# Performance work log

Hardware: AMD Instinct MI355X
Metric: run time of the kernel (lower is better)

## Reference

```python
import jax, jax.numpy as jnp
import numpy as np

NU, NI, D, C, V, E, L = 100000, 50000, 128, 5, 200000, 200000, 10


def setup_inputs() -> dict:
    key = jax.random.key(0)
    ks = jax.random.split(key, 16)
    s = lambda fan_in: 1.0 / np.sqrt(fan_in)
    return {
        "urf": jax.random.normal(ks[0], (NU, D), jnp.float32),
        "irf": jax.random.normal(ks[1], (NI, D), jnp.float32),
        "utf": jax.random.normal(ks[2], (NU, D), jnp.float32),
        "itf": jax.random.normal(ks[3], (NI, D), jnp.float32),
        "w1r": jax.random.normal(ks[4], (2 * D, D), jnp.float32) * s(2 * D),
        "w2r": jax.random.normal(ks[5], (D, D), jnp.float32) * s(D),
        "w1t": jax.random.normal(ks[6], (2 * D, D), jnp.float32) * s(2 * D),
        "w2t": jax.random.normal(ks[7], (D, D), jnp.float32) * s(D),
        "wp": jax.random.normal(ks[8], (D, C), jnp.float32) * s(D),
        "emb": jax.random.normal(ks[9], (V, D), jnp.float32),
        "src": jax.random.randint(ks[10], (E,), 0, NU, jnp.int32),
        "dst": jax.random.randint(ks[11], (E,), 0, NI, jnp.int32),
        "sentence_id": jax.random.randint(ks[12], (E, L), 0, V, jnp.int32),
        "neg_sid": jax.random.randint(ks[13], (E, L), 1, V, jnp.int32),
    }


def _review_feature(emb, sid):
    # masked mean-pool of sentence embeddings: [E, L] -> [E, D]
    length = (sid > 0).astype(jnp.float32).sum(axis=-1, keepdims=True) + 1e-9
    return emb[sid].sum(axis=-2) / length


def reference(urf, irf, utf, itf, w1r, w2r, w1t, w2t, wp, emb,
              src, dst, sentence_id, neg_sid):
    # edge-wise gather of src (user) / dst (item) features + concat  [E, 2D]
    rf = jnp.concatenate([urf[src], irf[dst]], axis=1)
    rh = jax.nn.relu(rf @ w1r) @ w2r                      # rating_linear  [E, D]
    pr = rh @ wp                                          # rating_predictor [E, C]
    tf = jnp.concatenate([utf[src], itf[dst]], axis=1)
    th = jax.nn.relu(tf @ w1t) @ w2t + rh                 # topic_linear + residual
    pos_review = _review_feature(emb, sentence_id)        # [E, D]
    neg_review = _review_feature(emb, neg_sid)            # [E, D]
    pos_score = (th * pos_review).sum(axis=1)             # [E]
    neg_score = (th * neg_review).sum(axis=1)
    loss = -jax.nn.log_sigmoid(pos_score - neg_score)     # -log(sigmoid(pos-neg))
    return pr, loss.mean(), loss.mean()
```

## Files before the change

### kernel.cpp

```cpp
#include <hip/hip_runtime.h>

#define NU_ 100000
#define NI_ 50000
#define D_  128
#define C_  5
#define V_  200000
#define E_  200000
#define L_  10

typedef __bf16 bf16x8 __attribute__((ext_vector_type(8)));
typedef unsigned short u16;
typedef u16 u16x8 __attribute__((ext_vector_type(8)));
typedef float f32x4 __attribute__((ext_vector_type(4)));

#define W1R_OFF 0
#define W2R_OFF 32768
#define W1T_OFF 49152
#define W2T_OFF 81920
#define WTOT    98304
#define EMB_BYTE_OFF (256 * 1024)
#define EMB_ELEMS    (V_ * D_)

__device__ __forceinline__ u16 f2bf(float x) {
    union { float f; unsigned int u; } v; v.f = x;
    unsigned int u = v.u;
    return (u16)((u + 0x7FFFu + ((u >> 16) & 1u)) >> 16);
}
__device__ __forceinline__ float bfhi(unsigned int u) {
    union { unsigned int u; float f; } v; v.u = u & 0xFFFF0000u; return v.f;
}
__device__ __forceinline__ float bflo(unsigned int u) {
    union { unsigned int u; float f; } v; v.u = u << 16; return v.f;
}

__global__ void prep_kernel(const float* __restrict__ w1r, const float* __restrict__ w2r,
                            const float* __restrict__ w1t, const float* __restrict__ w2t,
                            u16* __restrict__ wbuf, float* __restrict__ loss_acc) {
    int idx = blockIdx.x * blockDim.x + threadIdx.x;
    if (idx == 0) *loss_acc = 0.f;
    if (idx >= WTOT) return;
    const float* src; int base;
    if (idx < W2R_OFF)      { src = w1r; base = W1R_OFF; }
    else if (idx < W1T_OFF) { src = w2r; base = W2R_OFF; }
    else if (idx < W2T_OFF) { src = w1t; base = W1T_OFF; }
    else                    { src = w2t; base = W2T_OFF; }
    int local = idx - base;
    int j = local & 7;
    int g = local >> 3;
    int n = g & 127;
    int kq = g >> 7;
    wbuf[idx] = f2bf(src[(kq * 8 + j) * 128 + n]);
}

__global__ void cvt_kernel(const float* __restrict__ src, u16* __restrict__ dst, int n8) {
    int i = blockIdx.x * blockDim.x + threadIdx.x;
    if (i >= n8) return;
    float4 a = *(const float4*)(src + (size_t)i * 8);
    float4 b = *(const float4*)(src + (size_t)i * 8 + 4);
    u16x8 v;
    v[0] = f2bf(a.x); v[1] = f2bf(a.y); v[2] = f2bf(a.z); v[3] = f2bf(a.w);
    v[4] = f2bf(b.x); v[5] = f2bf(b.y); v[6] = f2bf(b.z); v[7] = f2bf(b.w);
    *(u16x8*)(dst + (size_t)i * 8) = v;
}

__device__ __forceinline__ void stage_half(const float* __restrict__ row, int lane, u16* buf) {
    int m = lane >> 2, q = lane & 3;
    const float* seg = row + q * 32;
#pragma unroll
    for (int i = 0; i < 4; i++) {
        float4 a = *(const float4*)(seg + i * 8);
        float4 b = *(const float4*)(seg + i * 8 + 4);
        u16x8 v;
        v[0] = f2bf(a.x); v[1] = f2bf(a.y); v[2] = f2bf(a.z); v[3] = f2bf(a.w);
        v[4] = f2bf(b.x); v[5] = f2bf(b.y); v[6] = f2bf(b.z); v[7] = f2bf(b.w);
        *(u16x8*)(buf + ((q * 4 + i) * 16 + m) * 8) = v;
    }
}

template <int KT>
__device__ __forceinline__ void gemm_tile(const u16* aLDS, const u16* __restrict__ Wg,
                                          int lq, int ln, f32x4 acc[8]) {
#pragma unroll
    for (int kt = 0; kt < KT; kt++) {
        bf16x8 af = *(const bf16x8*)(aLDS + ((kt * 4 + lq) * 16 + ln) * 8);
#pragma unroll
        for (int nt = 0; nt < 8; nt++) {
            bf16x8 bfv = *(const bf16x8*)(Wg + (size_t)((kt * 4 + lq) * 128 + nt * 16 + ln) * 8);
            acc[nt] = __builtin_amdgcn_mfma_f32_16x16x32_bf16(af, bfv, acc[nt], 0, 0, 0);
        }
    }
}

__device__ __forceinline__ void store_h_relu(const f32x4 acc[8], u16* buf, int lq, int ln) {
#pragma unroll
    for (int nt = 0; nt < 8; nt++)
#pragma unroll
        for (int reg = 0; reg < 4; reg++) {
            float h = fmaxf(acc[nt][reg], 0.f);
            int dcol = nt * 16 + ln;
            int r = lq * 4 + reg;
            buf[((dcol >> 3) * 16 + r) * 8 + (dcol & 7)] = f2bf(h);
        }
}

__device__ __forceinline__ void mlp(const float* __restrict__ uF, const float* __restrict__ iF,
                                    const int* __restrict__ srcI, const int* __restrict__ dstI,
                                    int ebase, int lane, int lq, int ln,
                                    const u16* __restrict__ w1, const u16* __restrict__ w2,
                                    u16* bufA, u16* bufB, f32x4 acc[8]) {
    int e = ebase + (lane >> 2);
    int su = srcI[e], sd = dstI[e];
    f32x4 h1[8];
#pragma unroll
    for (int nt = 0; nt < 8; nt++) h1[nt] = (f32x4){0.f, 0.f, 0.f, 0.f};

    stage_half(uF + (size_t)su * D_, lane, bufA);
    __syncthreads();
    gemm_tile<4>(bufA, w1, lq, ln, h1);
    __syncthreads();
    stage_half(iF + (size_t)sd * D_, lane, bufA);
    __syncthreads();
    gemm_tile<4>(bufA, w1 + 16384, lq, ln, h1);
    store_h_relu(h1, bufB, lq, ln);
    __syncthreads();
    gemm_tile<4>(bufB, w2, lq, ln, acc);
}

__device__ __forceinline__ float softplus_(float x) {
    return fmaxf(x, 0.f) + log1pf(expf(-fabsf(x)));
}

template <bool EB>
__global__ __launch_bounds__(256, 3) void fused_kernel(
    const float* __restrict__ urf, const float* __restrict__ irf,
    const float* __restrict__ utf, const float* __restrict__ itf,
    const float* __restrict__ wp, const float* __restrict__ emb,
    const u16* __restrict__ embB,
    const int* __restrict__ srcI, const int* __restrict__ dstI,
    const int* __restrict__ sidI, const int* __restrict__ nsidI,
    const u16* __restrict__ wbuf, float* __restrict__ loss_acc,
    float* __restrict__ out) {
    __shared__ u16 smem[4 * 4096];
    const int tid = threadIdx.x;
    const int w = tid >> 6;
    const int lane = tid & 63;
    const int lq = lane >> 4;
    const int ln = lane & 15;
    u16* bufA = smem + w * 4096;
    u16* bufB = bufA + 2048;
    const int ebase = blockIdx.x * 64 + w * 16;

    f32x4 rh[8];
#pragma unroll
    for (int nt = 0; nt < 8; nt++) rh[nt] = (f32x4){0.f, 0.f, 0.f, 0.f};
    mlp(urf, irf, srcI, dstI, ebase, lane, lq, ln,
        wbuf + W1R_OFF, wbuf + W2R_OFF, bufA, bufB, rh);

    {
        float pp[4][5];
#pragma unroll
        for (int r = 0; r < 4; r++)
#pragma unroll
            for (int c = 0; c < 5; c++) pp[r][c] = 0.f;
#pragma unroll
        for (int nt = 0; nt < 8; nt++) {
            int d = nt * 16 + ln;
            float wpc[5];
#pragma unroll
            for (int c = 0; c < 5; c++) wpc[c] = wp[d * 5 + c];
#pragma unroll
            for (int reg = 0; reg < 4; reg++)
#pragma unroll
                for (int c = 0; c < 5; c++) pp[reg][c] += rh[nt][reg] * wpc[c];
        }
#pragma unroll
        for (int off = 1; off < 16; off <<= 1)
#pragma unroll
            for (int reg = 0; reg < 4; reg++)
#pragma unroll
                for (int c = 0; c < 5; c++)
                    pp[reg][c] += __shfl_xor(pp[reg][c], off, 64);
        if (ln == 0) {
#pragma unroll
            for (int reg = 0; reg < 4; reg++) {
                int e = ebase + lq * 4 + reg;
#pragma unroll
                for (int c = 0; c < 5; c++) out[(size_t)e * 5 + c] = pp[reg][c];
            }
        }
    }

    __syncthreads();
    f32x4 th[8];
#pragma unroll
    for (int nt = 0; nt < 8; nt++) th[nt] = rh[nt];
    mlp(utf, itf, srcI, dstI, ebase, lane, lq, ln,
        wbuf + W1T_OFF, wbuf + W2T_OFF, bufA, bufB, th);

    __syncthreads();
    float* thb = (float*)bufA;
    if constexpr (EB) {
#pragma unroll
        for (int nt = 0; nt < 8; nt++)
#pragma unroll
            for (int reg = 0; reg < 4; reg++) {
                int col = nt * 16 + ln;
                thb[((lq * 4 + reg) * 16 + (col >> 3)) * 8 + (col & 7)] = th[nt][reg];
            }
    } else {
#pragma unroll
        for (int nt = 0; nt < 8; nt++)
#pragma unroll
            for (int reg = 0; reg < 4; reg++)
                thb[(lq * 4 + reg) * 128 + nt * 16 + ln] = th[nt][reg];
    }
    __syncthreads();

    float wave_loss = 0.f;
    if constexpr (EB) {
        const int g = lane >> 4, gl = lane & 15;
        for (int it = 0; it < 4; it++) {
            int m = it * 4 + g;
            int e = ebase + m;
            float th8[8];
            *(f32x4*)th8       = *(const f32x4*)(thb + (m * 16 + gl) * 8);
            *(f32x4*)(th8 + 4) = *(const f32x4*)(thb + (m * 16 + gl) * 8 + 4);
            float ps = 0.f, ns = 0.f;
            int pcnt = 0, ncnt = 0;
#pragma unroll
            for (int i = 0; i < L_; i++) {
                int s = sidI[e * L_ + i];
                pcnt += (s > 0) ? 1 : 0;
                union { u16x8 v; unsigned int u[4]; } cv;
                cv.v = *(const u16x8*)(embB + (size_t)s * D_ + gl * 8);
#pragma unroll
                for (int k = 0; k < 4; k++) {
                    ps = fmaf(th8[2 * k],     bflo(cv.u[k]), ps);
                    ps = fmaf(th8[2 * k + 1], bfhi(cv.u[k]), ps);
                }
            }
#pragma unroll
            for (int i = 0; i < L_; i++) {
                int s = nsidI[e * L_ + i];
                ncnt += (s > 0) ? 1 : 0;
                union { u16x8 v; unsigned int u[4]; } cv;
                cv.v = *(const u16x8*)(embB + (size_t)s * D_ + gl * 8);
#pragma unroll
                for (int k = 0; k < 4; k++) {
                    ns = fmaf(th8[2 * k],     bflo(cv.u[k]), ns);
                    ns = fmaf(th8[2 * k + 1], bfhi(cv.u[k]), ns);
                }
            }
#pragma unroll
            for (int off = 1; off < 16; off <<= 1) {
                ps += __shfl_xor(ps, off, 64);
                ns += __shfl_xor(ns, off, 64);
            }
            if (gl == 0) {
                ps /= ((float)pcnt + 1e-9f);
                ns /= ((float)ncnt + 1e-9f);
                wave_loss += softplus_(ns - ps);
            }
        }
        wave_loss += __shfl_xor(wave_loss, 16, 64);
        wave_loss += __shfl_xor(wave_loss, 32, 64);
    } else {
        const int h = lane >> 5, hl = lane & 31;
        for (int mp = 0; mp < 16; mp += 2) {
            int m = mp + h;
            int e = ebase + m;
            float4 t4 = *(const float4*)(thb + m * 128 + hl * 4);
            float ps = 0.f, ns = 0.f;
            int pcnt = 0, ncnt = 0;
#pragma unroll
            for (int i = 0; i < L_; i++) {
                int s = sidI[e * L_ + i];
                pcnt += (s > 0) ? 1 : 0;
                float4 ev = *(const float4*)(emb + (size_t)s * D_ + hl * 4);
                ps += t4.x * ev.x + t4.y * ev.y + t4.z * ev.z + t4.w * ev.w;
            }
#pragma unroll
            for (int i = 0; i < L_; i++) {
                int s = nsidI[e * L_ + i];
                ncnt += (s > 0) ? 1 : 0;
                float4 ev = *(const float4*)(emb + (size_t)s * D_ + hl * 4);
                ns += t4.x * ev.x + t4.y * ev.y + t4.z * ev.z + t4.w * ev.w;
            }
#pragma unroll
            for (int off = 1; off < 32; off <<= 1) {
                ps += __shfl_xor(ps, off, 64);
                ns += __shfl_xor(ns, off, 64);
            }
            if (hl == 0) {
                ps /= ((float)pcnt + 1e-9f);
                ns /= ((float)ncnt + 1e-9f);
                wave_loss += softplus_(ns - ps);
            }
        }
        wave_loss += __shfl_xor(wave_loss, 32, 64);
    }
    if (lane == 0) atomicAdd(loss_acc, wave_loss);
}

__global__ void finish_kernel(const float* __restrict__ loss_acc, float* __restrict__ out) {
    float v = loss_acc[0] * (1.0f / (float)E_);
    out[(size_t)E_ * C_]     = v;
    out[(size_t)E_ * C_ + 1] = v;
}

extern "C" void kernel_launch(void* const* d_in, const int* in_sizes, int n_in,
                              void* d_out, int out_size, void* d_ws, size_t ws_size,
                              hipStream_t stream) {
    const float* urf = (const float*)d_in[0];
    const float* irf = (const float*)d_in[1];
    const float* utf = (const float*)d_in[2];
    const float* itf = (const float*)d_in[3];
    const float* w1r = (const float*)d_in[4];
    const float* w2r = (const float*)d_in[5];
    const float* w1t = (const float*)d_in[6];
    const float* w2t = (const float*)d_in[7];
    const float* wp  = (const float*)d_in[8];
    const float* emb = (const float*)d_in[9];
    const int* srcI  = (const int*)d_in[10];
    const int* dstI  = (const int*)d_in[11];
    const int* sidI  = (const int*)d_in[12];
    const int* nsidI = (const int*)d_in[13];
    float* out = (float*)d_out;

    float* loss_acc = (float*)d_ws;
    u16* wbuf = (u16*)((char*)d_ws + 256);
    u16* embB = (u16*)((char*)d_ws + EMB_BYTE_OFF);

    bool eb = ws_size >= (size_t)EMB_BYTE_OFF + (size_t)EMB_ELEMS * 2;

    prep_kernel<<<(WTOT + 255) / 256, 256, 0, stream>>>(w1r, w2r, w1t, w2t, wbuf, loss_acc);
    if (eb)
        cvt_kernel<<<(EMB_ELEMS / 8 + 255) / 256, 256, 0, stream>>>(emb, embB, EMB_ELEMS / 8);

    if (eb)
        fused_kernel<true><<<E_ / 64, 256, 0, stream>>>(
            urf, irf, utf, itf, wp, emb, embB,
            srcI, dstI, sidI, nsidI, wbuf, loss_acc, out);
    else
        fused_kernel<false><<<E_ / 64, 256, 0, stream>>>(
            urf, irf, utf, itf, wp, emb, embB,
            srcI, dstI, sidI, nsidI, wbuf, loss_acc, out);

    finish_kernel<<<1, 1, 0, stream>>>(loss_acc, out);
}
```

Before: 588.9 us.

## Split fused kernel into MLP kernel and review-scoring kernel via bf16 th buffer

Splits the single fused kernel into two. The first runs both MLPs and the rating predictor and writes th to a workspace buffer in bf16. The second gathers sentence embeddings with 16 lanes per edge and computes the pos/neg scores and the loss. The split lets each stage use its own occupancy (3 vs 8 blocks per CU) and parallel layout for the latency-bound embedding gathers. In exchange it adds a global round trip for th and rounds th to bf16 before the dot products. It runs only when the workspace is large enough for both buffers.

```diff
diff --git a/kernel.cpp b/kernel.cpp
--- a/kernel.cpp
+++ b/kernel.cpp
@@ -20,6 +20,8 @@
 #define WTOT    98304
 #define EMB_BYTE_OFF (256 * 1024)
 #define EMB_ELEMS    (V_ * D_)
+#define TH_BYTE_OFF  (EMB_BYTE_OFF + EMB_ELEMS * 2)
+#define TH_BYTES     ((size_t)E_ * D_ * 2)
 
 __device__ __forceinline__ u16 f2bf(float x) {
     union { float f; unsigned int u; } v; v.f = x;
@@ -128,6 +130,152 @@
 
 __device__ __forceinline__ float softplus_(float x) {
     return fmaxf(x, 0.f) + log1pf(expf(-fabsf(x)));
+}
+
+
+__global__ __launch_bounds__(256, 3) void mlp_kernel(
+    const float* __restrict__ urf, const float* __restrict__ irf,
+    const float* __restrict__ utf, const float* __restrict__ itf,
+    const float* __restrict__ wp,
+    const int* __restrict__ srcI, const int* __restrict__ dstI,
+    const u16* __restrict__ wbuf, float* __restrict__ out,
+    u16* __restrict__ thB) {
+    __shared__ u16 smem[4 * 4096];
+    const int tid = threadIdx.x;
+    const int w = tid >> 6;
+    const int lane = tid & 63;
+    const int lq = lane >> 4;
+    const int ln = lane & 15;
+    u16* bufA = smem + w * 4096;
+    u16* bufB = bufA + 2048;
+    const int ebase = blockIdx.x * 64 + w * 16;
+
+    f32x4 rh[8];
+#pragma unroll
+    for (int nt = 0; nt < 8; nt++) rh[nt] = (f32x4){0.f, 0.f, 0.f, 0.f};
+    mlp(urf, irf, srcI, dstI, ebase, lane, lq, ln,
+        wbuf + W1R_OFF, wbuf + W2R_OFF, bufA, bufB, rh);
+
+    {
+        float pp[4][5];
+#pragma unroll
+        for (int r = 0; r < 4; r++)
+#pragma unroll
+            for (int c = 0; c < 5; c++) pp[r][c] = 0.f;
+#pragma unroll
+        for (int nt = 0; nt < 8; nt++) {
+            int d = nt * 16 + ln;
+            float wpc[5];
+#pragma unroll
+            for (int c = 0; c < 5; c++) wpc[c] = wp[d * 5 + c];
+#pragma unroll
+            for (int reg = 0; reg < 4; reg++)
+#pragma unroll
+                for (int c = 0; c < 5; c++) pp[reg][c] += rh[nt][reg] * wpc[c];
+        }
+#pragma unroll
+        for (int off = 1; off < 16; off <<= 1)
+#pragma unroll
+            for (int reg = 0; reg < 4; reg++)
+#pragma unroll
+                for (int c = 0; c < 5; c++)
+                    pp[reg][c] += __shfl_xor(pp[reg][c], off, 64);
+        if (ln == 0) {
+#pragma unroll
+            for (int reg = 0; reg < 4; reg++) {
+                int e = ebase + lq * 4 + reg;
+#pragma unroll
+                for (int c = 0; c < 5; c++) out[(size_t)e * 5 + c] = pp[reg][c];
+            }
+        }
+    }
+
+    __syncthreads();
+    f32x4 th[8];
+#pragma unroll
+    for (int nt = 0; nt < 8; nt++) th[nt] = rh[nt];
+    mlp(utf, itf, srcI, dstI, ebase, lane, lq, ln,
+        wbuf + W1T_OFF, wbuf + W2T_OFF, bufA, bufB, th);
+
+    __syncthreads();
+    float* thb = (float*)bufA;
+#pragma unroll
+    for (int nt = 0; nt < 8; nt++)
+#pragma unroll
+        for (int reg = 0; reg < 4; reg++)
+            thb[(lq * 4 + reg) * 128 + nt * 16 + ln] = th[nt][reg];
+    __syncthreads();
+
+#pragma unroll
+    for (int m = 0; m < 16; m++) {
+        float2 ab = *(const float2*)(thb + m * 128 + lane * 2);
+        unsigned pk = (unsigned)f2bf(ab.x) | ((unsigned)f2bf(ab.y) << 16);
+        ((unsigned*)(thB + (size_t)(ebase + m) * D_))[lane] = pk;
+    }
+}
+
+__global__ __launch_bounds__(256, 8) void review_kernel(
+    const u16* __restrict__ thB, const u16* __restrict__ embB,
+    const int* __restrict__ sidI, const int* __restrict__ nsidI,
+    float* __restrict__ loss_acc) {
+    __shared__ float red[4];
+    const int tid = threadIdx.x;
+    const int lane = tid & 63;
+    const int gl = tid & 15;
+    const int e = blockIdx.x * 16 + (tid >> 4);
+
+    int ip = 0, in_ = 0;
+    if (gl < L_) { ip = sidI[e * L_ + gl]; in_ = nsidI[e * L_ + gl]; }
+
+    float th8[8];
+    {
+        union { u16x8 v; unsigned int u[4]; } tu;
+        tu.v = *(const u16x8*)(thB + (size_t)e * D_ + gl * 8);
+#pragma unroll
+        for (int k = 0; k < 4; k++) {
+            th8[2 * k]     = bflo(tu.u[k]);
+            th8[2 * k + 1] = bfhi(tu.u[k]);
+        }
+    }
+
+    float ps = 0.f, ns = 0.f;
+    float pc = (gl < L_ && ip > 0) ? 1.f : 0.f;
+    float nc = (gl < L_ && in_ > 0) ? 1.f : 0.f;
+
+#pragma unroll
+    for (int i = 0; i < L_; i++) {
+        int s = __shfl(ip, i, 16);
+        union { u16x8 v; unsigned int u[4]; } cv;
+        cv.v = *(const u16x8*)(embB + (size_t)s * D_ + gl * 8);
+        int t = __shfl(in_, i, 16);
+        union { u16x8 v; unsigned int u[4]; } nv;
+        nv.v = *(const u16x8*)(embB + (size_t)t * D_ + gl * 8);
+#pragma unroll
+        for (int k = 0; k < 4; k++) {
+            ps = fmaf(th8[2 * k],     bflo(cv.u[k]), ps);
+            ps = fmaf(th8[2 * k + 1], bfhi(cv.u[k]), ps);
+        }
+#pragma unroll
+        for (int k = 0; k < 4; k++) {
+            ns = fmaf(th8[2 * k],     bflo(nv.u[k]), ns);
+            ns = fmaf(th8[2 * k + 1], bfhi(nv.u[k]), ns);
+        }
+    }
+
+#pragma unroll
+    for (int off = 1; off < 16; off <<= 1) {
+        ps += __shfl_xor(ps, off, 64);
+        ns += __shfl_xor(ns, off, 64);
+        pc += __shfl_xor(pc, off, 64);
+        nc += __shfl_xor(nc, off, 64);
+    }
+    float val = softplus_(ns / (nc + 1e-9f) - ps / (pc + 1e-9f));
+    float wl = (gl == 0) ? val : 0.f;
+    wl += __shfl_xor(wl, 16, 64);
+    wl += __shfl_xor(wl, 32, 64);
+    if (lane == 0) red[tid >> 6] = wl;
+    __syncthreads();
+    if (tid == 0) atomicAdd(loss_acc, red[0] + red[1] + red[2] + red[3]);
 }
 
 template <bool EB>
@@ -330,21 +478,29 @@
     float* loss_acc = (float*)d_ws;
     u16* wbuf = (u16*)((char*)d_ws + 256);
     u16* embB = (u16*)((char*)d_ws + EMB_BYTE_OFF);
+    u16* thB  = (u16*)((char*)d_ws + TH_BYTE_OFF);
 
     bool eb = ws_size >= (size_t)EMB_BYTE_OFF + (size_t)EMB_ELEMS * 2;
+    bool tb = ws_size >= (size_t)TH_BYTE_OFF + TH_BYTES;
 
     prep_kernel<<<(WTOT + 255) / 256, 256, 0, stream>>>(w1r, w2r, w1t, w2t, wbuf, loss_acc);
     if (eb)
         cvt_kernel<<<(EMB_ELEMS / 8 + 255) / 256, 256, 0, stream>>>(emb, embB, EMB_ELEMS / 8);
 
-    if (eb)
+    if (tb) {
+        mlp_kernel<<<E_ / 64, 256, 0, stream>>>(
+            urf, irf, utf, itf, wp, srcI, dstI, wbuf, out, thB);
+        review_kernel<<<E_ / 16, 256, 0, stream>>>(
+            thB, embB, sidI, nsidI, loss_acc);
+    } else if (eb) {
         fused_kernel<true><<<E_ / 64, 256, 0, stream>>>(
             urf, irf, utf, itf, wp, emb, embB,
             srcI, dstI, sidI, nsidI, wbuf, loss_acc, out);
-    else
+    } else {
         fused_kernel<false><<<E_ / 64, 256, 0, stream>>>(
             urf, irf, utf, itf, wp, emb, embB,
             srcI, dstI, sidI, nsidI, wbuf, loss_acc, out);
+    }
 
     finish_kernel<<<1, 1, 0, stream>>>(loss_acc, out);
 }
```

Measured after the change: 611.6 us. 3.9% more time.
